# Kernel optimization log

Hardware: AMD Instinct MI355X
Metric: run time of the kernel (lower is better)

The kernel has to match this reference:

```python
import jax, jax.numpy as jnp
import numpy as np
import math

B, N, D = 16, 1024, 1024

def setup_inputs() -> dict:
    key = jax.random.key(0)
    k1, k2, k3, k4 = jax.random.split(key, 4)
    x = jax.random.normal(k1, (B, N, D), dtype=jnp.float32)
    # Keras 'random_normal' initializer defaults to stddev=0.05
    w_keys = jax.random.normal(k2, (N, N), dtype=jnp.float32) * 0.05
    w_queries = jax.random.normal(k3, (N, N), dtype=jnp.float32) * 0.05
    w_values = jax.random.normal(k4, (N, N), dtype=jnp.float32) * 0.05
    return {"x": x, "w_keys": w_keys, "w_queries": w_queries, "w_values": w_values}

def reference(x, w_keys, w_queries, w_values):
    # x: (B, N, D); weights: (N, N); fact = sqrt(N) per build(input_shape[1])
    fact = math.sqrt(x.shape[1])
    ip = jnp.swapaxes(x, 1, 2)              # (B, D, N)
    vk = ip @ w_keys                         # (B, D, N)
    vq = ip @ w_queries                      # (B, D, N)
    vv = ip @ w_values                       # (B, D, N)
    kq = jnp.einsum('bdn,ben->bde', vk, vq) / fact   # (B, D, D)
    sm = jax.nn.softmax(kq, axis=-1)         # softmax over last axis
    # tf: sm @ transpose(pm(vv)) == sm @ vv  since pm then transpose_b cancel
    out = jnp.einsum('bde,ben->bdn', sm, vv) # (B, D, N)
    return jnp.swapaxes(out, 1, 2)           # (B, N, D)
```

## Files before the change

kernel.cpp:

```cpp
#include <hip/hip_runtime.h>
#include <stdint.h>


typedef __bf16 bf16x8_t __attribute__((ext_vector_type(8)));
typedef float  f32x4_t  __attribute__((ext_vector_type(4)));

typedef __attribute__((address_space(3))) uint32_t as3_u32;
typedef __attribute__((address_space(1))) uint32_t as1_u32;

__device__ __forceinline__ void async_copy16(const void* g, const void* l) {
  __builtin_amdgcn_global_load_lds((const as1_u32*)(uintptr_t)g,
                                   (as3_u32*)(uint32_t)(uintptr_t)l,
                                   16, 0, 0);
}

__device__ __forceinline__ uint16_t f2bf(float f) {
  uint32_t x = __float_as_uint(f);
  return (uint16_t)((x + 0x7fffu + ((x >> 16) & 1u)) >> 16);
}
__device__ __forceinline__ float bf2f(uint16_t b) {
  return __uint_as_float(((uint32_t)b) << 16);
}

template <int EPI>
__global__ __launch_bounds__(512, 2)
void gemm_bt256(const uint16_t* __restrict__ A, const uint16_t* __restrict__ B,
                void* __restrict__ Cv, size_t sA, size_t sB, size_t sC,
                float alpha, float* __restrict__ Sp)
{
  __shared__ __align__(16) char smem[131072];

  const int lid  = blockIdx.x;
  const int xcd  = lid & 7;
  const int slot = lid >> 3;
  const int z    = (xcd << 1) | (slot >> 4);
  const int t16  = slot & 15;
  const int bm0  = (t16 >> 2) << 8;
  const int bn0  = (t16 & 3) << 8;

  A += (size_t)z * sA + ((size_t)bm0 << 10);
  B += (size_t)z * sB + ((size_t)bn0 << 10);

  const int t    = threadIdx.x;
  const int lane = t & 63;
  const int w    = t >> 6;
  const int q    = lane >> 4;
  const int r16  = lane & 15;
  const int wm   = (w >> 2) << 7;
  const int wn   = (w & 3) << 6;

  const int g0  = t >> 3;
  const int cp  = t & 7;
  const int ce  = (cp ^ (g0 & 7)) << 3;
  const int sAo = (g0 << 7) + (cp << 4);
  const int rB  = ((g0 >> 5) << 6) + (g0 & 31);
  const int sBo = (rB << 7) + (cp << 4);
  const uint16_t* Ab = A + ((size_t)g0 << 10) + ce;
  const uint16_t* Bb = B + ((size_t)rB << 10) + ce;

#define STAGE_A(s, kge, dst) do {                                              \
    async_copy16(Ab + (((s)*64 +   0) << 10) + (kge),                          \
                 smem + (dst) + sAo + (s)*8192);                               \
    async_copy16(Ab + (((s)*64 + 128) << 10) + (kge),                          \
                 smem + (dst) + sAo + (s)*8192 + 16384);                       \
  } while (0)
#define STAGE_B(s, kge, dst) do {                                              \
    async_copy16(Bb + (((s)*32 +   0) << 10) + (kge),                          \
                 smem + (dst) + 32768 + sBo + (s)*4096);                       \
    async_copy16(Bb + (((s)*32 + 128) << 10) + (kge),                          \
                 smem + (dst) + 32768 + sBo + (s)*4096 + 16384);               \
  } while (0)

  const int sl0 = ((0 + q) ^ (r16 & 7)) << 4;
  const int sl1 = ((4 + q) ^ (r16 & 7)) << 4;
  int aRd0 = ((wm + r16) << 7) + sl0;
  int aRd1 = ((wm + r16) << 7) + sl1;
  int bRd0 = 32768 + ((wn + r16) << 7) + sl0;
  int bRd1 = 32768 + ((wn + r16) << 7) + sl1;

  f32x4_t acc[8][4];
#pragma unroll
  for (int i = 0; i < 8; i++)
#pragma unroll
    for (int j = 0; j < 4; j++) acc[i][j] = (f32x4_t){0.f, 0.f, 0.f, 0.f};

  bf16x8_t afa[4][2], afb[4][2], bA[2][2], bB[2][2];

  STAGE_A(0, 0, 0);
  STAGE_B(0, 0, 0);
  STAGE_B(1, 0, 0);
  STAGE_A(1, 0, 0);
  asm volatile("s_waitcnt vmcnt(4)" ::: "memory");
  __builtin_amdgcn_s_barrier();
#pragma unroll
  for (int mi = 0; mi < 4; ++mi) {
    afa[mi][0] = *(const bf16x8_t*)(smem + aRd0 + mi * 2048);
    afa[mi][1] = *(const bf16x8_t*)(smem + aRd1 + mi * 2048);
  }
#pragma unroll
  for (int ni = 0; ni < 2; ++ni) {
    bA[ni][0] = *(const bf16x8_t*)(smem + bRd0 + ni * 2048);
    bA[ni][1] = *(const bf16x8_t*)(smem + bRd1 + ni * 2048);
  }

  int nxt = 65536;
  for (int t0 = 0; t0 < 16; ++t0) {
    const int kge = ((t0 + 1) & 15) << 6;

    STAGE_A(0, kge, nxt);
    STAGE_B(0, kge, nxt);
    asm volatile("s_waitcnt vmcnt(4)" ::: "memory");
    __builtin_amdgcn_s_barrier();
#pragma unroll
    for (int ni = 0; ni < 2; ++ni) {
      bB[ni][0] = *(const bf16x8_t*)(smem + bRd0 + 4096 + ni * 2048);
      bB[ni][1] = *(const bf16x8_t*)(smem + bRd1 + 4096 + ni * 2048);
    }
    __builtin_amdgcn_s_setprio(1);
#pragma unroll
    for (int kk = 0; kk < 2; ++kk)
#pragma unroll
      for (int mi = 0; mi < 4; ++mi)
#pragma unroll
        for (int ni = 0; ni < 2; ++ni)
          acc[mi][ni] = __builtin_amdgcn_mfma_f32_16x16x32_bf16(
              afa[mi][kk], bA[ni][kk], acc[mi][ni], 0, 0, 0);
    __builtin_amdgcn_s_setprio(0);
    __builtin_amdgcn_s_barrier();

    STAGE_B(1, kge, nxt);
    STAGE_A(1, kge, nxt);
    __builtin_amdgcn_s_barrier();
#pragma unroll
    for (int mi = 0; mi < 4; ++mi) {
      afb[mi][0] = *(const bf16x8_t*)(smem + aRd0 + 8192 + mi * 2048);
      afb[mi][1] = *(const bf16x8_t*)(smem + aRd1 + 8192 + mi * 2048);
    }
    __builtin_amdgcn_s_setprio(1);
#pragma unroll
    for (int kk = 0; kk < 2; ++kk)
#pragma unroll
      for (int mi = 0; mi < 4; ++mi)
#pragma unroll
        for (int ni = 0; ni < 2; ++ni)
          acc[mi][2 + ni] = __builtin_amdgcn_mfma_f32_16x16x32_bf16(
              afa[mi][kk], bB[ni][kk], acc[mi][2 + ni], 0, 0, 0);
    __builtin_amdgcn_s_setprio(0);
    __builtin_amdgcn_s_barrier();

    __builtin_amdgcn_s_barrier();
    __builtin_amdgcn_s_setprio(1);
#pragma unroll
    for (int kk = 0; kk < 2; ++kk)
#pragma unroll
      for (int mi = 0; mi < 4; ++mi)
#pragma unroll
        for (int ni = 0; ni < 2; ++ni)
          acc[4 + mi][2 + ni] = __builtin_amdgcn_mfma_f32_16x16x32_bf16(
              afb[mi][kk], bB[ni][kk], acc[4 + mi][2 + ni], 0, 0, 0);
    __builtin_amdgcn_s_setprio(0);
    __builtin_amdgcn_s_barrier();

    asm volatile("s_waitcnt vmcnt(4)" ::: "memory");
    __builtin_amdgcn_s_barrier();
    __builtin_amdgcn_s_setprio(1);
#pragma unroll
    for (int kk = 0; kk < 2; ++kk)
#pragma unroll
      for (int mi = 0; mi < 4; ++mi)
#pragma unroll
        for (int ni = 0; ni < 2; ++ni)
          acc[4 + mi][ni] = __builtin_amdgcn_mfma_f32_16x16x32_bf16(
              afb[mi][kk], bA[ni][kk], acc[4 + mi][ni], 0, 0, 0);
    __builtin_amdgcn_s_setprio(0);
#pragma unroll
    for (int mi = 0; mi < 4; ++mi) {
      afa[mi][0] = *(const bf16x8_t*)(smem + (aRd0 ^ 65536) + mi * 2048);
      afa[mi][1] = *(const bf16x8_t*)(smem + (aRd1 ^ 65536) + mi * 2048);
    }
#pragma unroll
    for (int ni = 0; ni < 2; ++ni) {
      bA[ni][0] = *(const bf16x8_t*)(smem + (bRd0 ^ 65536) + ni * 2048);
      bA[ni][1] = *(const bf16x8_t*)(smem + (bRd1 ^ 65536) + ni * 2048);
    }
    __builtin_amdgcn_s_barrier();

    aRd0 ^= 65536; aRd1 ^= 65536; bRd0 ^= 65536; bRd1 ^= 65536; nxt ^= 65536;
  }
#undef STAGE_A
#undef STAGE_B

  asm volatile("s_waitcnt vmcnt(0)" ::: "memory");
  __builtin_amdgcn_s_barrier();

  if constexpr (EPI == 3) {
    float inv[4];
#pragma unroll
    for (int ni = 0; ni < 4; ++ni) {
      const int c = bn0 + wn + (ni << 4) + r16;
      float S = 0.f;
#pragma unroll
      for (int p = 0; p < 16; ++p)
        S += Sp[((size_t)p << 14) + ((size_t)z << 10) + c];
      inv[ni] = 1.0f / S;
    }
    float* C = (float*)Cv + (size_t)z * sC;
#pragma unroll
    for (int mi = 0; mi < 8; ++mi)
#pragma unroll
      for (int ni = 0; ni < 4; ++ni)
#pragma unroll
        for (int r = 0; r < 4; ++r) {
          const int row = bm0 + wm + (mi << 4) + (q << 2) + r;
          const int col = bn0 + wn + (ni << 4) + r16;
          C[((size_t)row << 10) + col] = acc[mi][ni][r] * alpha * inv[ni];
        }
  } else {
    float* reg = (float*)smem + (size_t)w * 1056;
    uint16_t* C = (uint16_t*)Cv + (size_t)z * sC;
    float* SpW = Sp + ((size_t)(((bn0 >> 8) << 2) + (w & 3)) << 14)
                    + ((size_t)z << 10);
#pragma unroll
    for (int mi = 0; mi < 8; ++mi) {
      if constexpr (EPI == 2) {
        float ev[4][4];
#pragma unroll
        for (int ni = 0; ni < 4; ++ni)
#pragma unroll
          for (int r = 0; r < 4; ++r) {
            ev[ni][r] = __expf(acc[mi][ni][r] * alpha);
            reg[((q << 2) + r) * 66 + (ni << 4) + r16] = ev[ni][r];
          }
#pragma unroll
        for (int r = 0; r < 4; ++r) {
          float s = ev[0][r] + ev[1][r] + ev[2][r] + ev[3][r];
          s += __shfl_xor(s, 1, 16);
          s += __shfl_xor(s, 2, 16);
          s += __shfl_xor(s, 4, 16);
          s += __shfl_xor(s, 8, 16);
          if (r16 == 0)
            SpW[bm0 + wm + (mi << 4) + (q << 2) + r] = s;
        }
      } else {
#pragma unroll
        for (int ni = 0; ni < 4; ++ni)
#pragma unroll
          for (int r = 0; r < 4; ++r)
            reg[((q << 2) + r) * 66 + (ni << 4) + r16] = acc[mi][ni][r] * alpha;
      }
#pragma unroll
      for (int it = 0; it < 8; ++it) {
        const int rr = (it << 1) + (lane >> 5);
        const int cc = (lane & 31) << 1;
        const float2 v = *(const float2*)(reg + rr * 66 + cc);
        const uint32_t p = (uint32_t)f2bf(v.x) | ((uint32_t)f2bf(v.y) << 16);
        const int row = bm0 + wm + (mi << 4) + rr;
        const int col = bn0 + wn + cc;
        *(uint32_t*)(C + ((size_t)row << 10) + col) = p;
      }
    }
  }
}

__global__ __launch_bounds__(256, 4)
void gemm128_splitk(const uint16_t* __restrict__ A, const uint16_t* __restrict__ B,
                    float* __restrict__ P)
{
  __shared__ __align__(16) char smem[32768];
  char* As = smem;
  char* Bs = smem + 16384;

  const int slice = blockIdx.x >> 6;
  const int tile  = blockIdx.x & 63;
  const int bm0   = (tile >> 3) << 7;
  const int bn0   = (tile & 7) << 7;
  const int koff  = slice << 8;

  const int t    = threadIdx.x;
  const int lane = t & 63;
  const int w    = t >> 6;
  const int q    = lane >> 4;
  const int r16  = lane & 15;
  const int wm   = (w >> 1) << 6;
  const int wn   = (w & 1) << 6;

  f32x4_t acc[4][4];
#pragma unroll
  for (int i = 0; i < 4; i++)
#pragma unroll
    for (int j = 0; j < 4; j++) acc[i][j] = (f32x4_t){0.f, 0.f, 0.f, 0.f};

  for (int k0 = koff; k0 < koff + 256; k0 += 64) {
#pragma unroll
    for (int i = 0; i < 4; i++) {
      const int o  = (i << 12) + (t << 4);
      const int m  = o >> 7;
      const int cp = (o >> 4) & 7;
      const int c  = cp ^ (m & 7);
      async_copy16(A + (size_t)(bm0 + m) * 1024 + (size_t)(k0 + (c << 3)), As + o);
      async_copy16(B + (size_t)(bn0 + m) * 1024 + (size_t)(k0 + (c << 3)), Bs + o);
    }
    __syncthreads();
#pragma unroll
    for (int kk = 0; kk < 2; kk++) {
      bf16x8_t af[4], bfr[4];
#pragma unroll
      for (int mi = 0; mi < 4; mi++) {
        const int m = wm + (mi << 4) + r16;
        const int c = (kk << 2) + q;
        af[mi] = *(const bf16x8_t*)(As + (m << 7) + ((c ^ (m & 7)) << 4));
      }
#pragma unroll
      for (int ni = 0; ni < 4; ni++) {
        const int n = wn + (ni << 4) + r16;
        const int c = (kk << 2) + q;
        bfr[ni] = *(const bf16x8_t*)(Bs + (n << 7) + ((c ^ (n & 7)) << 4));
      }
#pragma unroll
      for (int mi = 0; mi < 4; mi++)
#pragma unroll
        for (int ni = 0; ni < 4; ni++)
          acc[mi][ni] = __builtin_amdgcn_mfma_f32_16x16x32_bf16(
              af[mi], bfr[ni], acc[mi][ni], 0, 0, 0);
    }
    __syncthreads();
  }

  float* C = P + (size_t)slice * (1024u * 1024u);
#pragma unroll
  for (int mi = 0; mi < 4; mi++)
#pragma unroll
    for (int ni = 0; ni < 4; ni++)
#pragma unroll
      for (int r = 0; r < 4; r++) {
        const int row = bm0 + wm + (mi << 4) + (q << 2) + r;
        const int col = bn0 + wn + (ni << 4) + r16;
        C[((size_t)row << 10) + col] = acc[mi][ni][r];
      }
}

__global__ __launch_bounds__(256)
void reduce_w2t(const float* __restrict__ P, uint16_t* __restrict__ W)
{
  const size_t i4 = (((size_t)blockIdx.x << 8) + threadIdx.x) << 2;
  const float4 a = *(const float4*)(P + i4);
  const float4 b = *(const float4*)(P + (1u << 20) + i4);
  const float4 c = *(const float4*)(P + (2u << 20) + i4);
  const float4 d = *(const float4*)(P + (3u << 20) + i4);
  ushort4 r;
  r.x = f2bf(a.x + b.x + c.x + d.x);
  r.y = f2bf(a.y + b.y + c.y + d.y);
  r.z = f2bf(a.z + b.z + c.z + d.z);
  r.w = f2bf(a.w + b.w + c.w + d.w);
  *(ushort4*)(W + i4) = r;
}

__global__ __launch_bounds__(256)
void prep_w(const float* __restrict__ w0, const float* __restrict__ w1,
            const float* __restrict__ w2, uint16_t* __restrict__ o0,
            uint16_t* __restrict__ o1, uint16_t* __restrict__ o2)
{
  __shared__ float tile[32][33];
  const int z = blockIdx.z;
  const int c0 = blockIdx.x << 5;
  const int r0 = blockIdx.y << 5;
  const int tx = threadIdx.x;
  const int ty = threadIdx.y;
  if (z < 2) {
    const float* src = z ? w1 : w0;
    uint16_t* dst = z ? o1 : o0;
#pragma unroll
    for (int i = 0; i < 32; i += 8)
      dst[(size_t)(r0 + ty + i) * 1024 + (c0 + tx)] =
          f2bf(src[(size_t)(r0 + ty + i) * 1024 + (c0 + tx)]);
  } else {
#pragma unroll
    for (int i = 0; i < 32; i += 8)
      tile[ty + i][tx] = w2[(size_t)(r0 + ty + i) * 1024 + (c0 + tx)];
    __syncthreads();
#pragma unroll
    for (int i = 0; i < 32; i += 8)
      o2[(size_t)(c0 + ty + i) * 1024 + (r0 + tx)] = f2bf(tile[tx][ty + i]);
  }
}

__global__ __launch_bounds__(256)
void transpose_cast(const float* __restrict__ src, uint16_t* __restrict__ dst,
                    int R, int Ccols, size_t sStride, size_t dStride)
{
  __shared__ float tile[32][33];
  const int z = blockIdx.z;
  src += (size_t)z * sStride;
  dst += (size_t)z * dStride;
  const int c0 = blockIdx.x << 5;
  const int r0 = blockIdx.y << 5;
  const int tx = threadIdx.x;
  const int ty = threadIdx.y;
#pragma unroll
  for (int i = 0; i < 32; i += 8)
    tile[ty + i][tx] = src[(size_t)(r0 + ty + i) * Ccols + (c0 + tx)];
  __syncthreads();
#pragma unroll
  for (int i = 0; i < 32; i += 8)
    dst[(size_t)(c0 + ty + i) * R + (r0 + tx)] = f2bf(tile[tx][ty + i]);
}

extern "C" void kernel_launch(void* const* d_in, const int* in_sizes, int n_in,
                              void* d_out, int out_size, void* d_ws, size_t ws_size,
                              hipStream_t stream)
{
  const float* x  = (const float*)d_in[0];
  const float* wk = (const float*)d_in[1];
  const float* wq = (const float*)d_in[2];
  const float* wv = (const float*)d_in[3];
  float* out = (float*)d_out;

  constexpr int BB = 16, N = 1024, D = 1024;
  constexpr size_t DN = (size_t)D * N;

  char* ws = (char*)d_ws;
  uint16_t* xT   = (uint16_t*)(ws);
  uint16_t* Wkc  = (uint16_t*)(ws + (32ull << 20));
  uint16_t* Wqc  = (uint16_t*)(ws + (34ull << 20));
  uint16_t* Wtv  = (uint16_t*)(ws + (36ull << 20));
  uint16_t* W2Tc = (uint16_t*)(ws + (38ull << 20));
  float*    W2p  = (float*)   (ws + (40ull << 20));
  uint16_t* tmp  = (uint16_t*)(ws + (56ull << 20));
  uint16_t* vvT  = (uint16_t*)(ws + (88ull << 20));
  uint16_t* P    = (uint16_t*)(ws + (120ull << 20));
  float*    Spart= (float*)   (ws + (152ull << 20));

  const dim3 tb(32, 8);
  prep_w<<<dim3(N / 32, N / 32, 3), tb, 0, stream>>>(wk, wq, wv, Wkc, Wqc, Wtv);
  gemm128_splitk<<<256, 256, 0, stream>>>(Wqc, Wkc, W2p);
  reduce_w2t<<<1024, 256, 0, stream>>>(W2p, W2Tc);
  transpose_cast<<<dim3(D / 32, N / 32, BB), tb, 0, stream>>>(x, xT, N, D, DN, DN);
  gemm_bt256<0><<<256, 512, 0, stream>>>(xT, W2Tc, tmp, DN, 0, DN, 1.0f, Spart);
  gemm_bt256<0><<<256, 512, 0, stream>>>(Wtv, xT, vvT, 0, DN, DN, 1.0f, Spart);
  gemm_bt256<2><<<256, 512, 0, stream>>>(tmp, xT, P, DN, DN, DN, 0.03125f, Spart);
  gemm_bt256<3><<<256, 512, 0, stream>>>(vvT, P, out, DN, DN, DN, 1.0f, Spart);
}
```

Before: 291.7 us.

## Replace pipelined 256x256 GEMM with simpler 256x128 tile kernel at higher occupancy

The hand-pipelined 256x256 bf16 MFMA GEMM, which double-buffers 128KB of LDS, is replaced by a 256x128 tile kernel. The new kernel uses a single 48KB LDS buffer, a plain load/sync/compute loop, and a 512-block grid. The aim is more resident blocks per CU and more blocks than CUs, so that occupancy hides memory latency instead of explicit software pipelining. The softmax partial-sum indexing is updated for 16 column partials per row. In exchange, there is no load/compute overlap within a block, less operand reuse per tile, and a risk of register spills under the tighter launch bound.

Result: faster. 282.5 us (-3.2%).

```diff
diff --git a/kernel.cpp b/kernel.cpp
--- a/kernel.cpp
+++ b/kernel.cpp
@@ -23,20 +23,23 @@
 }
 
 template <int EPI>
-__global__ __launch_bounds__(512, 2)
-void gemm_bt256(const uint16_t* __restrict__ A, const uint16_t* __restrict__ B,
-                void* __restrict__ Cv, size_t sA, size_t sB, size_t sC,
-                float alpha, float* __restrict__ Sp)
-{
-  __shared__ __align__(16) char smem[131072];
+__global__ __launch_bounds__(512, 4)
+void gemm_bt256x128(const uint16_t* __restrict__ A,
+                    const uint16_t* __restrict__ B,
+                    void* __restrict__ Cv, size_t sA, size_t sB, size_t sC,
+                    float alpha, float* __restrict__ Sp)
+{
+  __shared__ __align__(16) char smem[49152];
+  char* As = smem;
+  char* Bs = smem + 32768;
 
   const int lid  = blockIdx.x;
   const int xcd  = lid & 7;
   const int slot = lid >> 3;
-  const int z    = (xcd << 1) | (slot >> 4);
-  const int t16  = slot & 15;
-  const int bm0  = (t16 >> 2) << 8;
-  const int bn0  = (t16 & 3) << 8;
+  const int z    = (xcd << 1) | (slot >> 5);
+  const int t32  = slot & 31;
+  const int bm0  = (t32 >> 3) << 8;
+  const int bn0  = (t32 & 7) << 7;
 
   A += (size_t)z * sA + ((size_t)bm0 << 10);
   B += (size_t)z * sB + ((size_t)bn0 << 10);
@@ -46,152 +49,57 @@
   const int w    = t >> 6;
   const int q    = lane >> 4;
   const int r16  = lane & 15;
-  const int wm   = (w >> 2) << 7;
-  const int wn   = (w & 3) << 6;
+  const int wm   = (w >> 1) << 6;
+  const int wn   = (w & 1) << 6;
 
   const int g0  = t >> 3;
   const int cp  = t & 7;
   const int ce  = (cp ^ (g0 & 7)) << 3;
-  const int sAo = (g0 << 7) + (cp << 4);
-  const int rB  = ((g0 >> 5) << 6) + (g0 & 31);
-  const int sBo = (rB << 7) + (cp << 4);
-  const uint16_t* Ab = A + ((size_t)g0 << 10) + ce;
-  const uint16_t* Bb = B + ((size_t)rB << 10) + ce;
-
-#define STAGE_A(s, kge, dst) do {                                              \
-    async_copy16(Ab + (((s)*64 +   0) << 10) + (kge),                          \
-                 smem + (dst) + sAo + (s)*8192);                               \
-    async_copy16(Ab + (((s)*64 + 128) << 10) + (kge),                          \
-                 smem + (dst) + sAo + (s)*8192 + 16384);                       \
-  } while (0)
-#define STAGE_B(s, kge, dst) do {                                              \
-    async_copy16(Bb + (((s)*32 +   0) << 10) + (kge),                          \
-                 smem + (dst) + 32768 + sBo + (s)*4096);                       \
-    async_copy16(Bb + (((s)*32 + 128) << 10) + (kge),                          \
-                 smem + (dst) + 32768 + sBo + (s)*4096 + 16384);               \
-  } while (0)
-
-  const int sl0 = ((0 + q) ^ (r16 & 7)) << 4;
-  const int sl1 = ((4 + q) ^ (r16 & 7)) << 4;
-  int aRd0 = ((wm + r16) << 7) + sl0;
-  int aRd1 = ((wm + r16) << 7) + sl1;
-  int bRd0 = 32768 + ((wn + r16) << 7) + sl0;
-  int bRd1 = 32768 + ((wn + r16) << 7) + sl1;
-
-  f32x4_t acc[8][4];
-#pragma unroll
-  for (int i = 0; i < 8; i++)
+  const int so  = (g0 << 7) + (cp << 4);
+  const uint16_t* Ag = A + ((size_t)g0 << 10) + ce;
+  const uint16_t* Bg = B + ((size_t)g0 << 10) + ce;
+
+  f32x4_t acc[4][4];
+#pragma unroll
+  for (int i = 0; i < 4; i++)
 #pragma unroll
     for (int j = 0; j < 4; j++) acc[i][j] = (f32x4_t){0.f, 0.f, 0.f, 0.f};
 
-  bf16x8_t afa[4][2], afb[4][2], bA[2][2], bB[2][2];
-
-  STAGE_A(0, 0, 0);
-  STAGE_B(0, 0, 0);
-  STAGE_B(1, 0, 0);
-  STAGE_A(1, 0, 0);
-  asm volatile("s_waitcnt vmcnt(4)" ::: "memory");
-  __builtin_amdgcn_s_barrier();
-#pragma unroll
-  for (int mi = 0; mi < 4; ++mi) {
-    afa[mi][0] = *(const bf16x8_t*)(smem + aRd0 + mi * 2048);
-    afa[mi][1] = *(const bf16x8_t*)(smem + aRd1 + mi * 2048);
+  for (int k0 = 0; k0 < 1024; k0 += 64) {
+#pragma unroll
+    for (int s = 0; s < 4; ++s)
+      async_copy16(Ag + (((size_t)s << 6) << 10) + k0, As + so + (s << 13));
+#pragma unroll
+    for (int s = 0; s < 2; ++s)
+      async_copy16(Bg + (((size_t)s << 6) << 10) + k0, Bs + so + (s << 13));
+    __syncthreads();
+
+#pragma unroll
+    for (int kk = 0; kk < 2; ++kk) {
+      bf16x8_t af[4], bfr[4];
+#pragma unroll
+      for (int mi = 0; mi < 4; ++mi) {
+        const int m = wm + (mi << 4) + r16;
+        const int c = (kk << 2) + q;
+        af[mi] = *(const bf16x8_t*)(As + (m << 7) + ((c ^ (m & 7)) << 4));
+      }
+#pragma unroll
+      for (int ni = 0; ni < 4; ++ni) {
+        const int n = wn + (ni << 4) + r16;
+        const int c = (kk << 2) + q;
+        bfr[ni] = *(const bf16x8_t*)(Bs + (n << 7) + ((c ^ (n & 7)) << 4));
+      }
+      __builtin_amdgcn_s_setprio(1);
+#pragma unroll
+      for (int mi = 0; mi < 4; ++mi)
+#pragma unroll
+        for (int ni = 0; ni < 4; ++ni)
+          acc[mi][ni] = __builtin_amdgcn_mfma_f32_16x16x32_bf16(
+              af[mi], bfr[ni], acc[mi][ni], 0, 0, 0);
+      __builtin_amdgcn_s_setprio(0);
+    }
+    __syncthreads();
   }
-#pragma unroll
-  for (int ni = 0; ni < 2; ++ni) {
-    bA[ni][0] = *(const bf16x8_t*)(smem + bRd0 + ni * 2048);
-    bA[ni][1] = *(const bf16x8_t*)(smem + bRd1 + ni * 2048);
-  }
-
-  int nxt = 65536;
-  for (int t0 = 0; t0 < 16; ++t0) {
-    const int kge = ((t0 + 1) & 15) << 6;
-
-    STAGE_A(0, kge, nxt);
-    STAGE_B(0, kge, nxt);
-    asm volatile("s_waitcnt vmcnt(4)" ::: "memory");
-    __builtin_amdgcn_s_barrier();
-#pragma unroll
-    for (int ni = 0; ni < 2; ++ni) {
-      bB[ni][0] = *(const bf16x8_t*)(smem + bRd0 + 4096 + ni * 2048);
-      bB[ni][1] = *(const bf16x8_t*)(smem + bRd1 + 4096 + ni * 2048);
-    }
-    __builtin_amdgcn_s_setprio(1);
-#pragma unroll
-    for (int kk = 0; kk < 2; ++kk)
-#pragma unroll
-      for (int mi = 0; mi < 4; ++mi)
-#pragma unroll
-        for (int ni = 0; ni < 2; ++ni)
-          acc[mi][ni] = __builtin_amdgcn_mfma_f32_16x16x32_bf16(
-              afa[mi][kk], bA[ni][kk], acc[mi][ni], 0, 0, 0);
-    __builtin_amdgcn_s_setprio(0);
-    __builtin_amdgcn_s_barrier();
-
-    STAGE_B(1, kge, nxt);
-    STAGE_A(1, kge, nxt);
-    __builtin_amdgcn_s_barrier();
-#pragma unroll
-    for (int mi = 0; mi < 4; ++mi) {
-      afb[mi][0] = *(const bf16x8_t*)(smem + aRd0 + 8192 + mi * 2048);
-      afb[mi][1] = *(const bf16x8_t*)(smem + aRd1 + 8192 + mi * 2048);
-    }
-    __builtin_amdgcn_s_setprio(1);
-#pragma unroll
-    for (int kk = 0; kk < 2; ++kk)
-#pragma unroll
-      for (int mi = 0; mi < 4; ++mi)
-#pragma unroll
-        for (int ni = 0; ni < 2; ++ni)
-          acc[mi][2 + ni] = __builtin_amdgcn_mfma_f32_16x16x32_bf16(
-              afa[mi][kk], bB[ni][kk], acc[mi][2 + ni], 0, 0, 0);
-    __builtin_amdgcn_s_setprio(0);
-    __builtin_amdgcn_s_barrier();
-
-    __builtin_amdgcn_s_barrier();
-    __builtin_amdgcn_s_setprio(1);
-#pragma unroll
-    for (int kk = 0; kk < 2; ++kk)
-#pragma unroll
-      for (int mi = 0; mi < 4; ++mi)
-#pragma unroll
-        for (int ni = 0; ni < 2; ++ni)
-          acc[4 + mi][2 + ni] = __builtin_amdgcn_mfma_f32_16x16x32_bf16(
-              afb[mi][kk], bB[ni][kk], acc[4 + mi][2 + ni], 0, 0, 0);
-    __builtin_amdgcn_s_setprio(0);
-    __builtin_amdgcn_s_barrier();
-
-    asm volatile("s_waitcnt vmcnt(4)" ::: "memory");
-    __builtin_amdgcn_s_barrier();
-    __builtin_amdgcn_s_setprio(1);
-#pragma unroll
-    for (int kk = 0; kk < 2; ++kk)
-#pragma unroll
-      for (int mi = 0; mi < 4; ++mi)
-#pragma unroll
-        for (int ni = 0; ni < 2; ++ni)
-          acc[4 + mi][ni] = __builtin_amdgcn_mfma_f32_16x16x32_bf16(
-              afb[mi][kk], bA[ni][kk], acc[4 + mi][ni], 0, 0, 0);
-    __builtin_amdgcn_s_setprio(0);
-#pragma unroll
-    for (int mi = 0; mi < 4; ++mi) {
-      afa[mi][0] = *(const bf16x8_t*)(smem + (aRd0 ^ 65536) + mi * 2048);
-      afa[mi][1] = *(const bf16x8_t*)(smem + (aRd1 ^ 65536) + mi * 2048);
-    }
-#pragma unroll
-    for (int ni = 0; ni < 2; ++ni) {
-      bA[ni][0] = *(const bf16x8_t*)(smem + (bRd0 ^ 65536) + ni * 2048);
-      bA[ni][1] = *(const bf16x8_t*)(smem + (bRd1 ^ 65536) + ni * 2048);
-    }
-    __builtin_amdgcn_s_barrier();
-
-    aRd0 ^= 65536; aRd1 ^= 65536; bRd0 ^= 65536; bRd1 ^= 65536; nxt ^= 65536;
-  }
-#undef STAGE_A
-#undef STAGE_B
-
-  asm volatile("s_waitcnt vmcnt(0)" ::: "memory");
-  __builtin_amdgcn_s_barrier();
 
   if constexpr (EPI == 3) {
     float inv[4];
@@ -206,7 +114,7 @@
     }
     float* C = (float*)Cv + (size_t)z * sC;
 #pragma unroll
-    for (int mi = 0; mi < 8; ++mi)
+    for (int mi = 0; mi < 4; ++mi)
 #pragma unroll
       for (int ni = 0; ni < 4; ++ni)
 #pragma unroll
@@ -218,10 +126,10 @@
   } else {
     float* reg = (float*)smem + (size_t)w * 1056;
     uint16_t* C = (uint16_t*)Cv + (size_t)z * sC;
-    float* SpW = Sp + ((size_t)(((bn0 >> 8) << 2) + (w & 3)) << 14)
+    float* SpW = Sp + ((size_t)(((bn0 >> 7) << 1) + (w & 1)) << 14)
                     + ((size_t)z << 10);
 #pragma unroll
-    for (int mi = 0; mi < 8; ++mi) {
+    for (int mi = 0; mi < 4; ++mi) {
       if constexpr (EPI == 2) {
         float ev[4][4];
 #pragma unroll
@@ -435,8 +343,8 @@
   gemm128_splitk<<<256, 256, 0, stream>>>(Wqc, Wkc, W2p);
   reduce_w2t<<<1024, 256, 0, stream>>>(W2p, W2Tc);
   transpose_cast<<<dim3(D / 32, N / 32, BB), tb, 0, stream>>>(x, xT, N, D, DN, DN);
-  gemm_bt256<0><<<256, 512, 0, stream>>>(xT, W2Tc, tmp, DN, 0, DN, 1.0f, Spart);
-  gemm_bt256<0><<<256, 512, 0, stream>>>(Wtv, xT, vvT, 0, DN, DN, 1.0f, Spart);
-  gemm_bt256<2><<<256, 512, 0, stream>>>(tmp, xT, P, DN, DN, DN, 0.03125f, Spart);
-  gemm_bt256<3><<<256, 512, 0, stream>>>(vvT, P, out, DN, DN, DN, 1.0f, Spart);
-}
+  gemm_bt256x128<0><<<512, 512, 0, stream>>>(xT, W2Tc, tmp, DN, 0, DN, 1.0f, Spart);
+  gemm_bt256x128<0><<<512, 512, 0, stream>>>(Wtv, xT, vvT, 0, DN, DN, 1.0f, Spart);
+  gemm_bt256x128<2><<<512, 512, 0, stream>>>(tmp, xT, P, DN, DN, DN, 0.03125f, Spart);
+  gemm_bt256x128<3><<<512, 512, 0, stream>>>(vvT, P, out, DN, DN, DN, 1.0f, Spart);
+}
```
